# Performance work log

Hardware: AMD Instinct MI355X
Metric: run time of the kernel (lower is better)

Reference implementation:

```python
import jax, jax.numpy as jnp
import numpy as np
from jax import lax

T = 1.0      # terminal time
SIGMA = 1.0  # diffusion coefficient
N, D, P, M, H = 16384, 16, 8, 50, 128


def setup_inputs() -> dict:
    key = jax.random.key(0)
    ks = jax.random.split(key, 8)
    scale1 = 1.0 / np.sqrt(1 + D + P)
    scale2 = 1.0 / np.sqrt(H)
    return {
        "initial_states": jax.random.normal(ks[0], (N, D), jnp.float32),
        "initial_values": jax.random.normal(ks[1], (N,), jnp.float32),
        "observations": jax.random.normal(ks[2], (N, P), jnp.float32),
        "noise": jax.random.normal(ks[3], (M, N, D), jnp.float32),
        "W1": jax.random.normal(ks[4], (1 + D + P, H), jnp.float32) * scale1,
        "b1": jnp.zeros((H,), jnp.float32),
        "W2": jax.random.normal(ks[5], (H, H), jnp.float32) * scale2,
        "b2": jnp.zeros((H,), jnp.float32),
        "W3": jax.random.normal(ks[6], (H, D), jnp.float32) * scale2,
        "b3": jnp.zeros((D,), jnp.float32),
    }


def reference(initial_states, initial_values, observations, noise,
              W1, b1, W2, b2, W3, b3):
    """Euler-Maruyama rollout of simulate_SDEs: joint (X, V) SDE with
    per-step Z-network drift. drift b(X) = -X (OU process)."""
    m_steps = noise.shape[0]
    dt = jnp.asarray(T / m_steps, initial_states.dtype)
    sqrt_dt = jnp.sqrt(dt)
    times = jnp.arange(m_steps, dtype=initial_states.dtype) * dt  # time[m]

    def z_net(t, X, Y):
        tcol = jnp.full((X.shape[0], 1), t, X.dtype)
        h = jnp.concatenate([tcol, X, Y], axis=1)      # (N, 1+d+p)
        h = jax.nn.relu(h @ W1 + b1)
        h = jax.nn.relu(h @ W2 + b2)
        return h @ W3 + b3                             # (N, d)

    def step(carry, inp):
        X, V = carry
        eps, t = inp
        Wn = sqrt_dt * eps                             # Brownian increment
        Z = z_net(t, X, observations)
        drift_V = 0.5 * jnp.sum(Z * Z, axis=1)
        V = V + dt * drift_V + jnp.sum(Z * Wn, axis=1)
        X = X + dt * (-X) + SIGMA * Wn                 # b(X) = -X
        return (X, V), None

    (X, V), _ = lax.scan(step, (initial_states, initial_values), (noise, times))
    return X, V
```

## Files before the change

### kernel.cpp

```cpp
#include <hip/hip_runtime.h>

typedef __bf16   bf16x8 __attribute__((ext_vector_type(8)));
typedef float    f32x4  __attribute__((ext_vector_type(4)));
typedef float    f32x2  __attribute__((ext_vector_type(2)));
typedef uint32_t u32x4  __attribute__((ext_vector_type(4)));

constexpr int N_ = 16384;
constexpr int D_ = 16;
constexpr int P_ = 8;
constexpr int H_ = 128;
constexpr int M_ = 50;

__device__ __forceinline__ uint32_t pk_bf16(float a, float b) {
    uint32_t ua = __builtin_bit_cast(uint32_t, a) + 0x8000u;
    uint32_t ub = __builtin_bit_cast(uint32_t, b) + 0x8000u;
    return __builtin_amdgcn_perm(ub, ua, 0x07060302u);
}
__device__ __forceinline__ uint32_t pk_relu_bf16(float a, float b) {
    return pk_bf16(fmaxf(a, 0.0f), fmaxf(b, 0.0f));
}

__global__ __launch_bounds__(64, 1)
void sde_fused(const float* __restrict__ X0,
               const float* __restrict__ V0,
               const float* __restrict__ Yobs,
               const float* __restrict__ noise,
               const float* __restrict__ W1, const float* __restrict__ b1,
               const float* __restrict__ W2, const float* __restrict__ b2,
               const float* __restrict__ W3, const float* __restrict__ b3,
               float* __restrict__ out)
{
    const int lane = threadIdx.x;
    const int n    = lane & 15;
    const int q    = lane >> 4;
    const int gr   = blockIdx.x * 16 + n;

    const float dt   = 0.02f;
    const float sqdt = 0.1414213562373095f;

    bf16x8 w1f[8];
#pragma unroll
    for (int ct = 0; ct < 8; ++ct) {
        u32x4 u;
        u[0] = pk_bf16(W1[(1 + q * 4 + 0) * H_ + ct * 16 + n],
                       W1[(1 + q * 4 + 1) * H_ + ct * 16 + n]);
        u[1] = pk_bf16(W1[(1 + q * 4 + 2) * H_ + ct * 16 + n],
                       W1[(1 + q * 4 + 3) * H_ + ct * 16 + n]);
        u[2] = pk_bf16(W1[(17 + q * 2 + 0) * H_ + ct * 16 + n],
                       W1[(17 + q * 2 + 1) * H_ + ct * 16 + n]);
        u[3] = (q == 0) ? pk_bf16(b1[ct * 16 + n], W1[ct * 16 + n]) : 0u;
        w1f[ct] = __builtin_bit_cast(bf16x8, u);
    }
    bf16x8 w2f[8][4];
#pragma unroll
    for (int ct = 0; ct < 8; ++ct)
#pragma unroll
        for (int kt = 0; kt < 4; ++kt) {
            u32x4 u;
#pragma unroll
            for (int w = 0; w < 4; ++w) {
                int h0 = (kt * 2 + (w >> 1)) * 16 + q * 4 + (w & 1) * 2;
                u[w] = pk_bf16(W2[h0 * H_ + ct * 16 + n],
                               W2[(h0 + 1) * H_ + ct * 16 + n]);
            }
            w2f[ct][kt] = __builtin_bit_cast(bf16x8, u);
        }
    bf16x8 w3f[4];
#pragma unroll
    for (int kt = 0; kt < 4; ++kt) {
        u32x4 u;
#pragma unroll
        for (int w = 0; w < 4; ++w) {
            int h0 = (kt * 2 + (w >> 1)) * 16 + q * 4 + (w & 1) * 2;
            u[w] = pk_bf16(W3[h0 * D_ + n], W3[(h0 + 1) * D_ + n]);
        }
        w3f[kt] = __builtin_bit_cast(bf16x8, u);
    }
    f32x4 b2r[8];
#pragma unroll
    for (int ct = 0; ct < 8; ++ct)
#pragma unroll
        for (int r = 0; r < 4; ++r) b2r[ct][r] = b2[ct * 16 + q * 4 + r];
    f32x4 b3r;
#pragma unroll
    for (int r = 0; r < 4; ++r) b3r[r] = b3[q * 4 + r];

    f32x4 x = *(const f32x4*)&X0[gr * D_ + q * 4];
    f32x2 y2 = *(const f32x2*)&Yobs[gr * P_ + q * 2];
    const uint32_t yw = pk_bf16(y2[0], y2[1]);

    const float* npb = noise + (size_t)gr * D_ + q * 4;
    f32x4 e0 = *(const f32x4*)npb;
    f32x4 e1 = *(const f32x4*)(npb + (size_t)N_ * D_);
    float t = 0.0f;
    float vacc = 0.0f;

    for (int m = 0; m < M_; ++m) {
        int mp = (m + 2 < M_) ? (m + 2) : (M_ - 1);
        f32x4 e2 = *(const f32x4*)(npb + (size_t)mp * N_ * D_);

        u32x4 au;
        au[0] = pk_bf16(x[0], x[1]);
        au[1] = pk_bf16(x[2], x[3]);
        au[2] = yw;
        au[3] = (q == 0) ? pk_bf16(1.0f, t) : 0u;
        bf16x8 a0 = __builtin_bit_cast(bf16x8, au);

        f32x4 h1c[8];
#pragma unroll
        for (int ct = 0; ct < 8; ++ct)
            h1c[ct] = __builtin_amdgcn_mfma_f32_16x16x32_bf16(
                w1f[ct], a0, (f32x4){0.f, 0.f, 0.f, 0.f}, 0, 0, 0);

        bf16x8 h1b[4];
#pragma unroll
        for (int kt = 0; kt < 4; ++kt) {
            u32x4 u;
            u[0] = pk_relu_bf16(h1c[2 * kt][0], h1c[2 * kt][1]);
            u[1] = pk_relu_bf16(h1c[2 * kt][2], h1c[2 * kt][3]);
            u[2] = pk_relu_bf16(h1c[2 * kt + 1][0], h1c[2 * kt + 1][1]);
            u[3] = pk_relu_bf16(h1c[2 * kt + 1][2], h1c[2 * kt + 1][3]);
            h1b[kt] = __builtin_bit_cast(bf16x8, u);
        }

        f32x4 h2c[8];
#pragma unroll
        for (int ct = 0; ct < 8; ++ct) {
            f32x4 c = b2r[ct];
#pragma unroll
            for (int kt = 0; kt < 4; ++kt)
                c = __builtin_amdgcn_mfma_f32_16x16x32_bf16(w2f[ct][kt], h1b[kt], c, 0, 0, 0);
            h2c[ct] = c;
        }
        bf16x8 h2b[4];
#pragma unroll
        for (int kt = 0; kt < 4; ++kt) {
            u32x4 u;
            u[0] = pk_relu_bf16(h2c[2 * kt][0], h2c[2 * kt][1]);
            u[1] = pk_relu_bf16(h2c[2 * kt][2], h2c[2 * kt][3]);
            u[2] = pk_relu_bf16(h2c[2 * kt + 1][0], h2c[2 * kt + 1][1]);
            u[3] = pk_relu_bf16(h2c[2 * kt + 1][2], h2c[2 * kt + 1][3]);
            h2b[kt] = __builtin_bit_cast(bf16x8, u);
        }

        f32x4 za = __builtin_amdgcn_mfma_f32_16x16x32_bf16(w3f[0], h2b[0], b3r, 0, 0, 0);
        za = __builtin_amdgcn_mfma_f32_16x16x32_bf16(w3f[1], h2b[1], za, 0, 0, 0);
        f32x4 zb = __builtin_amdgcn_mfma_f32_16x16x32_bf16(
            w3f[2], h2b[2], (f32x4){0.f, 0.f, 0.f, 0.f}, 0, 0, 0);
        zb = __builtin_amdgcn_mfma_f32_16x16x32_bf16(w3f[3], h2b[3], zb, 0, 0, 0);

#pragma unroll
        for (int r = 0; r < 4; ++r) {
            float z  = za[r] + zb[r];
            float wn = sqdt * e0[r];
            vacc = fmaf(z, wn, fmaf(0.01f * z, z, vacc));
            x[r] = fmaf(x[r], 0.98f, wn);
        }

        e0 = e1; e1 = e2;
        t += dt;
    }

    float part = vacc;
    part += __shfl_xor(part, 16);
    part += __shfl_xor(part, 32);
    float v = V0[gr] + part;

    *(f32x4*)&out[gr * D_ + q * 4] = x;
    if (q == 0) out[N_ * D_ + gr] = v;
}

extern "C" void kernel_launch(void* const* d_in, const int* in_sizes, int n_in,
                              void* d_out, int out_size, void* d_ws, size_t ws_size,
                              hipStream_t stream)
{
    const float* X0 = (const float*)d_in[0];
    const float* V0 = (const float*)d_in[1];
    const float* Y  = (const float*)d_in[2];
    const float* nz = (const float*)d_in[3];
    const float* W1 = (const float*)d_in[4];
    const float* b1 = (const float*)d_in[5];
    const float* W2 = (const float*)d_in[6];
    const float* b2 = (const float*)d_in[7];
    const float* W3 = (const float*)d_in[8];
    const float* b3 = (const float*)d_in[9];
    float* out = (float*)d_out;

    sde_fused<<<N_ / 16, 64, 0, stream>>>(X0, V0, Y, nz, W1, b1, W2, b2, W3, b3, out);
}
```

Measured before the change: 139.6 us.

## Interleave two Euler steps per iteration to overlap independent MFMA chains

Because the state update does not depend on the network output, the next step's state is computed up front. The MLPs for two consecutive timesteps are then issued together, giving the MFMA pipeline two independent dependency chains to hide latency with only one wave per block. It also replaces the manual bias-add bf16 packing with the hardware v_cvt_pk_bf16_f32 instruction. Costs include higher register use and slightly different rounding.

```diff
diff --git a/kernel.cpp b/kernel.cpp
--- a/kernel.cpp
+++ b/kernel.cpp
@@ -16,8 +16,13 @@
     uint32_t ub = __builtin_bit_cast(uint32_t, b) + 0x8000u;
     return __builtin_amdgcn_perm(ub, ua, 0x07060302u);
 }
-__device__ __forceinline__ uint32_t pk_relu_bf16(float a, float b) {
-    return pk_bf16(fmaxf(a, 0.0f), fmaxf(b, 0.0f));
+__device__ __forceinline__ uint32_t cvtpk(float a, float b) {
+    uint32_t r;
+    asm("v_cvt_pk_bf16_f32 %0, %1, %2" : "=v"(r) : "v"(a), "v"(b));
+    return r;
+}
+__device__ __forceinline__ uint32_t cvtpk_relu(float a, float b) {
+    return cvtpk(fmaxf(a, 0.0f), fmaxf(b, 0.0f));
 }
 
 __global__ __launch_bounds__(64, 1)
@@ -92,76 +97,131 @@
     const float* npb = noise + (size_t)gr * D_ + q * 4;
     f32x4 e0 = *(const f32x4*)npb;
     f32x4 e1 = *(const f32x4*)(npb + (size_t)N_ * D_);
-    float t = 0.0f;
-    float vacc = 0.0f;
-
-    for (int m = 0; m < M_; ++m) {
-        int mp = (m + 2 < M_) ? (m + 2) : (M_ - 1);
-        f32x4 e2 = *(const f32x4*)(npb + (size_t)mp * N_ * D_);
-
-        u32x4 au;
-        au[0] = pk_bf16(x[0], x[1]);
-        au[1] = pk_bf16(x[2], x[3]);
-        au[2] = yw;
-        au[3] = (q == 0) ? pk_bf16(1.0f, t) : 0u;
-        bf16x8 a0 = __builtin_bit_cast(bf16x8, au);
-
-        f32x4 h1c[8];
+    float vaccA = 0.0f, vaccB = 0.0f;
+
+#pragma unroll 1
+    for (int mm = 0; mm < M_; mm += 2) {
+        const int p0 = (mm + 2 < M_) ? (mm + 2) : (M_ - 1);
+        const int p1 = (mm + 3 < M_) ? (mm + 3) : (M_ - 1);
+        f32x4 eN0 = *(const f32x4*)(npb + (size_t)p0 * N_ * D_);
+        f32x4 eN1 = *(const f32x4*)(npb + (size_t)p1 * N_ * D_);
+
+        const float tA = (float)mm * dt;
+        const float tB = (float)(mm + 1) * dt;
+
+        f32x4 xB;
+#pragma unroll
+        for (int r = 0; r < 4; ++r) xB[r] = fmaf(x[r], 0.98f, sqdt * e0[r]);
+
+        u32x4 auA;
+        auA[0] = cvtpk(x[0], x[1]);
+        auA[1] = cvtpk(x[2], x[3]);
+        auA[2] = yw;
+        auA[3] = (q == 0) ? cvtpk(1.0f, tA) : 0u;
+        bf16x8 a0A = __builtin_bit_cast(bf16x8, auA);
+        u32x4 auB;
+        auB[0] = cvtpk(xB[0], xB[1]);
+        auB[1] = cvtpk(xB[2], xB[3]);
+        auB[2] = yw;
+        auB[3] = (q == 0) ? cvtpk(1.0f, tB) : 0u;
+        bf16x8 a0B = __builtin_bit_cast(bf16x8, auB);
+
+        f32x4 h1cA[8], h1cB[8];
 #pragma unroll
         for (int ct = 0; ct < 8; ++ct)
-            h1c[ct] = __builtin_amdgcn_mfma_f32_16x16x32_bf16(
-                w1f[ct], a0, (f32x4){0.f, 0.f, 0.f, 0.f}, 0, 0, 0);
-
-        bf16x8 h1b[4];
-#pragma unroll
-        for (int kt = 0; kt < 4; ++kt) {
-            u32x4 u;
-            u[0] = pk_relu_bf16(h1c[2 * kt][0], h1c[2 * kt][1]);
-            u[1] = pk_relu_bf16(h1c[2 * kt][2], h1c[2 * kt][3]);
-            u[2] = pk_relu_bf16(h1c[2 * kt + 1][0], h1c[2 * kt + 1][1]);
-            u[3] = pk_relu_bf16(h1c[2 * kt + 1][2], h1c[2 * kt + 1][3]);
-            h1b[kt] = __builtin_bit_cast(bf16x8, u);
-        }
-
-        f32x4 h2c[8];
+            h1cA[ct] = __builtin_amdgcn_mfma_f32_16x16x32_bf16(
+                w1f[ct], a0A, (f32x4){0.f, 0.f, 0.f, 0.f}, 0, 0, 0);
+#pragma unroll
+        for (int ct = 0; ct < 8; ++ct)
+            h1cB[ct] = __builtin_amdgcn_mfma_f32_16x16x32_bf16(
+                w1f[ct], a0B, (f32x4){0.f, 0.f, 0.f, 0.f}, 0, 0, 0);
+
+        bf16x8 h1bA[4], h1bB[4];
+#pragma unroll
+        for (int kt = 0; kt < 4; ++kt) {
+            u32x4 u;
+            u[0] = cvtpk_relu(h1cA[2 * kt][0], h1cA[2 * kt][1]);
+            u[1] = cvtpk_relu(h1cA[2 * kt][2], h1cA[2 * kt][3]);
+            u[2] = cvtpk_relu(h1cA[2 * kt + 1][0], h1cA[2 * kt + 1][1]);
+            u[3] = cvtpk_relu(h1cA[2 * kt + 1][2], h1cA[2 * kt + 1][3]);
+            h1bA[kt] = __builtin_bit_cast(bf16x8, u);
+        }
+#pragma unroll
+        for (int kt = 0; kt < 4; ++kt) {
+            u32x4 u;
+            u[0] = cvtpk_relu(h1cB[2 * kt][0], h1cB[2 * kt][1]);
+            u[1] = cvtpk_relu(h1cB[2 * kt][2], h1cB[2 * kt][3]);
+            u[2] = cvtpk_relu(h1cB[2 * kt + 1][0], h1cB[2 * kt + 1][1]);
+            u[3] = cvtpk_relu(h1cB[2 * kt + 1][2], h1cB[2 * kt + 1][3]);
+            h1bB[kt] = __builtin_bit_cast(bf16x8, u);
+        }
+
+        f32x4 h2cA[8], h2cB[8];
 #pragma unroll
         for (int ct = 0; ct < 8; ++ct) {
             f32x4 c = b2r[ct];
 #pragma unroll
             for (int kt = 0; kt < 4; ++kt)
-                c = __builtin_amdgcn_mfma_f32_16x16x32_bf16(w2f[ct][kt], h1b[kt], c, 0, 0, 0);
-            h2c[ct] = c;
-        }
-        bf16x8 h2b[4];
-#pragma unroll
-        for (int kt = 0; kt < 4; ++kt) {
-            u32x4 u;
-            u[0] = pk_relu_bf16(h2c[2 * kt][0], h2c[2 * kt][1]);
-            u[1] = pk_relu_bf16(h2c[2 * kt][2], h2c[2 * kt][3]);
-            u[2] = pk_relu_bf16(h2c[2 * kt + 1][0], h2c[2 * kt + 1][1]);
-            u[3] = pk_relu_bf16(h2c[2 * kt + 1][2], h2c[2 * kt + 1][3]);
-            h2b[kt] = __builtin_bit_cast(bf16x8, u);
-        }
-
-        f32x4 za = __builtin_amdgcn_mfma_f32_16x16x32_bf16(w3f[0], h2b[0], b3r, 0, 0, 0);
-        za = __builtin_amdgcn_mfma_f32_16x16x32_bf16(w3f[1], h2b[1], za, 0, 0, 0);
-        f32x4 zb = __builtin_amdgcn_mfma_f32_16x16x32_bf16(
-            w3f[2], h2b[2], (f32x4){0.f, 0.f, 0.f, 0.f}, 0, 0, 0);
-        zb = __builtin_amdgcn_mfma_f32_16x16x32_bf16(w3f[3], h2b[3], zb, 0, 0, 0);
+                c = __builtin_amdgcn_mfma_f32_16x16x32_bf16(
+                    w2f[ct][kt], h1bA[kt], c, 0, 0, 0);
+            h2cA[ct] = c;
+        }
+#pragma unroll
+        for (int ct = 0; ct < 8; ++ct) {
+            f32x4 c = b2r[ct];
+#pragma unroll
+            for (int kt = 0; kt < 4; ++kt)
+                c = __builtin_amdgcn_mfma_f32_16x16x32_bf16(
+                    w2f[ct][kt], h1bB[kt], c, 0, 0, 0);
+            h2cB[ct] = c;
+        }
+
+        bf16x8 h2bA[4], h2bB[4];
+#pragma unroll
+        for (int kt = 0; kt < 4; ++kt) {
+            u32x4 u;
+            u[0] = cvtpk_relu(h2cA[2 * kt][0], h2cA[2 * kt][1]);
+            u[1] = cvtpk_relu(h2cA[2 * kt][2], h2cA[2 * kt][3]);
+            u[2] = cvtpk_relu(h2cA[2 * kt + 1][0], h2cA[2 * kt + 1][1]);
+            u[3] = cvtpk_relu(h2cA[2 * kt + 1][2], h2cA[2 * kt + 1][3]);
+            h2bA[kt] = __builtin_bit_cast(bf16x8, u);
+        }
+#pragma unroll
+        for (int kt = 0; kt < 4; ++kt) {
+            u32x4 u;
+            u[0] = cvtpk_relu(h2cB[2 * kt][0], h2cB[2 * kt][1]);
+            u[1] = cvtpk_relu(h2cB[2 * kt][2], h2cB[2 * kt][3]);
+            u[2] = cvtpk_relu(h2cB[2 * kt + 1][0], h2cB[2 * kt + 1][1]);
+            u[3] = cvtpk_relu(h2cB[2 * kt + 1][2], h2cB[2 * kt + 1][3]);
+            h2bB[kt] = __builtin_bit_cast(bf16x8, u);
+        }
+
+        f32x4 zaA = __builtin_amdgcn_mfma_f32_16x16x32_bf16(w3f[0], h2bA[0], b3r, 0, 0, 0);
+        zaA = __builtin_amdgcn_mfma_f32_16x16x32_bf16(w3f[1], h2bA[1], zaA, 0, 0, 0);
+        f32x4 zbA = __builtin_amdgcn_mfma_f32_16x16x32_bf16(
+            w3f[2], h2bA[2], (f32x4){0.f, 0.f, 0.f, 0.f}, 0, 0, 0);
+        zbA = __builtin_amdgcn_mfma_f32_16x16x32_bf16(w3f[3], h2bA[3], zbA, 0, 0, 0);
+        f32x4 zaB = __builtin_amdgcn_mfma_f32_16x16x32_bf16(w3f[0], h2bB[0], b3r, 0, 0, 0);
+        zaB = __builtin_amdgcn_mfma_f32_16x16x32_bf16(w3f[1], h2bB[1], zaB, 0, 0, 0);
+        f32x4 zbB = __builtin_amdgcn_mfma_f32_16x16x32_bf16(
+            w3f[2], h2bB[2], (f32x4){0.f, 0.f, 0.f, 0.f}, 0, 0, 0);
+        zbB = __builtin_amdgcn_mfma_f32_16x16x32_bf16(w3f[3], h2bB[3], zbB, 0, 0, 0);
 
 #pragma unroll
         for (int r = 0; r < 4; ++r) {
-            float z  = za[r] + zb[r];
-            float wn = sqdt * e0[r];
-            vacc = fmaf(z, wn, fmaf(0.01f * z, z, vacc));
-            x[r] = fmaf(x[r], 0.98f, wn);
-        }
-
-        e0 = e1; e1 = e2;
-        t += dt;
+            float zA  = zaA[r] + zbA[r];
+            float wnA = sqdt * e0[r];
+            vaccA = fmaf(zA, wnA, fmaf(0.01f * zA, zA, vaccA));
+            float zB  = zaB[r] + zbB[r];
+            float wnB = sqdt * e1[r];
+            vaccB = fmaf(zB, wnB, fmaf(0.01f * zB, zB, vaccB));
+            x[r] = fmaf(xB[r], 0.98f, wnB);
+        }
+
+        e0 = eN0; e1 = eN1;
     }
 
-    float part = vacc;
+    float part = vaccA + vaccB;
     part += __shfl_xor(part, 16);
     part += __shfl_xor(part, 32);
     float v = V0[gr] + part;
```

Result: slower. 156.6 us (+12.2%).

## Stage W1/W3/b2 in LDS, interleave layer-2/3 MFMAs, use hardware bf16 convert

Applied to the files above, without the earlier changes.

Moves the W1 and W3 fragments and the b2 bias out of registers into shared memory and reloads them each step through volatile LDS reads just after use, so fewer values stay live. Layer-2 output is converted and fed into layer-3 MFMAs pair by pair instead of after all eight column tiles. Replaces the manual bit-rounding pack with the v_cvt_pk_bf16_f32 instruction and drops the two-step-ahead noise prefetch in favour of a load inside the non-unrolled loop. The aim is lower register pressure and better MFMA/convert overlap, at the cost of extra LDS traffic and noise-load latency now sitting on the per-step critical path.

```diff
diff --git a/kernel.cpp b/kernel.cpp
--- a/kernel.cpp
+++ b/kernel.cpp
@@ -16,8 +16,22 @@
     uint32_t ub = __builtin_bit_cast(uint32_t, b) + 0x8000u;
     return __builtin_amdgcn_perm(ub, ua, 0x07060302u);
 }
-__device__ __forceinline__ uint32_t pk_relu_bf16(float a, float b) {
-    return pk_bf16(fmaxf(a, 0.0f), fmaxf(b, 0.0f));
+__device__ __forceinline__ uint32_t cvtpk(float a, float b) {
+    uint32_t r;
+    asm("v_cvt_pk_bf16_f32 %0, %1, %2" : "=v"(r) : "v"(a), "v"(b));
+    return r;
+}
+__device__ __forceinline__ uint32_t cvtpk_relu(float a, float b) {
+    return cvtpk(fmaxf(a, 0.0f), fmaxf(b, 0.0f));
+}
+
+__device__ __forceinline__ bf16x8 lds_ldv8(const void* p) {
+    u32x4 v = *(volatile const u32x4*)p;
+    return __builtin_bit_cast(bf16x8, v);
+}
+__device__ __forceinline__ f32x4 lds_ldvf(const void* p) {
+    u32x4 v = *(volatile const u32x4*)p;
+    return __builtin_bit_cast(f32x4, v);
 }
 
 __global__ __launch_bounds__(64, 1)
@@ -38,7 +52,10 @@
     const float dt   = 0.02f;
     const float sqdt = 0.1414213562373095f;
 
-    bf16x8 w1f[8];
+    __shared__ bf16x8 w1s[8][64];
+    __shared__ bf16x8 w3s[4][64];
+    __shared__ float  b2s[H_];
+
 #pragma unroll
     for (int ct = 0; ct < 8; ++ct) {
         u32x4 u;
@@ -49,11 +66,23 @@
         u[2] = pk_bf16(W1[(17 + q * 2 + 0) * H_ + ct * 16 + n],
                        W1[(17 + q * 2 + 1) * H_ + ct * 16 + n]);
         u[3] = (q == 0) ? pk_bf16(b1[ct * 16 + n], W1[ct * 16 + n]) : 0u;
-        w1f[ct] = __builtin_bit_cast(bf16x8, u);
-    }
+        w1s[ct][lane] = __builtin_bit_cast(bf16x8, u);
+    }
+#pragma unroll
+    for (int kt = 0; kt < 4; ++kt) {
+        u32x4 u;
+#pragma unroll
+        for (int w = 0; w < 4; ++w) {
+            int h0 = (kt * 2 + (w >> 1)) * 16 + q * 4 + (w & 1) * 2;
+            u[w] = pk_bf16(W3[h0 * D_ + n], W3[(h0 + 1) * D_ + n]);
+        }
+        w3s[kt][lane] = __builtin_bit_cast(bf16x8, u);
+    }
+    if (lane < 32) *(f32x4*)&b2s[lane * 4] = *(const f32x4*)&b2[lane * 4];
+
     bf16x8 w2f[8][4];
 #pragma unroll
-    for (int ct = 0; ct < 8; ++ct)
+    for (int ct = 0; ct < 8; ++ct) {
 #pragma unroll
         for (int kt = 0; kt < 4; ++kt) {
             u32x4 u;
@@ -65,99 +94,102 @@
             }
             w2f[ct][kt] = __builtin_bit_cast(bf16x8, u);
         }
-    bf16x8 w3f[4];
-#pragma unroll
-    for (int kt = 0; kt < 4; ++kt) {
-        u32x4 u;
-#pragma unroll
-        for (int w = 0; w < 4; ++w) {
-            int h0 = (kt * 2 + (w >> 1)) * 16 + q * 4 + (w & 1) * 2;
-            u[w] = pk_bf16(W3[h0 * D_ + n], W3[(h0 + 1) * D_ + n]);
-        }
-        w3f[kt] = __builtin_bit_cast(bf16x8, u);
-    }
-    f32x4 b2r[8];
-#pragma unroll
-    for (int ct = 0; ct < 8; ++ct)
-#pragma unroll
-        for (int r = 0; r < 4; ++r) b2r[ct][r] = b2[ct * 16 + q * 4 + r];
-    f32x4 b3r;
-#pragma unroll
-    for (int r = 0; r < 4; ++r) b3r[r] = b3[q * 4 + r];
+        __builtin_amdgcn_sched_barrier(0);
+    }
+    f32x4 b3r = *(const f32x4*)&b3[q * 4];
+
+    __syncthreads();
 
     f32x4 x = *(const f32x4*)&X0[gr * D_ + q * 4];
     f32x2 y2 = *(const f32x2*)&Yobs[gr * P_ + q * 2];
     const uint32_t yw = pk_bf16(y2[0], y2[1]);
-
     const float* npb = noise + (size_t)gr * D_ + q * 4;
-    f32x4 e0 = *(const f32x4*)npb;
-    f32x4 e1 = *(const f32x4*)(npb + (size_t)N_ * D_);
+
+    bf16x8 w1buf[8];
+#pragma unroll
+    for (int k = 0; k < 8; ++k) w1buf[k] = lds_ldv8(&w1s[k][lane]);
+    bf16x8 w3buf[4];
+#pragma unroll
+    for (int k = 0; k < 4; ++k) w3buf[k] = lds_ldv8(&w3s[k][lane]);
+    f32x4 cb[4];
+    cb[0] = lds_ldvf(&b2s[0 * 16 + q * 4]);
+    cb[1] = lds_ldvf(&b2s[1 * 16 + q * 4]);
+
     float t = 0.0f;
     float vacc = 0.0f;
 
+#pragma unroll 1
     for (int m = 0; m < M_; ++m) {
-        int mp = (m + 2 < M_) ? (m + 2) : (M_ - 1);
-        f32x4 e2 = *(const f32x4*)(npb + (size_t)mp * N_ * D_);
+        f32x4 e = *(const f32x4*)(npb + (size_t)m * N_ * D_);
 
         u32x4 au;
-        au[0] = pk_bf16(x[0], x[1]);
-        au[1] = pk_bf16(x[2], x[3]);
+        au[0] = cvtpk(x[0], x[1]);
+        au[1] = cvtpk(x[2], x[3]);
         au[2] = yw;
-        au[3] = (q == 0) ? pk_bf16(1.0f, t) : 0u;
+        au[3] = (q == 0) ? cvtpk(1.0f, t) : 0u;
         bf16x8 a0 = __builtin_bit_cast(bf16x8, au);
 
-        f32x4 h1c[8];
-#pragma unroll
-        for (int ct = 0; ct < 8; ++ct)
-            h1c[ct] = __builtin_amdgcn_mfma_f32_16x16x32_bf16(
-                w1f[ct], a0, (f32x4){0.f, 0.f, 0.f, 0.f}, 0, 0, 0);
-
         bf16x8 h1b[4];
 #pragma unroll
         for (int kt = 0; kt < 4; ++kt) {
+            f32x4 ha = __builtin_amdgcn_mfma_f32_16x16x32_bf16(
+                w1buf[2 * kt], a0, (f32x4){0.f, 0.f, 0.f, 0.f}, 0, 0, 0);
+            f32x4 hb = __builtin_amdgcn_mfma_f32_16x16x32_bf16(
+                w1buf[2 * kt + 1], a0, (f32x4){0.f, 0.f, 0.f, 0.f}, 0, 0, 0);
+            w1buf[2 * kt]     = lds_ldv8(&w1s[2 * kt][lane]);
+            w1buf[2 * kt + 1] = lds_ldv8(&w1s[2 * kt + 1][lane]);
             u32x4 u;
-            u[0] = pk_relu_bf16(h1c[2 * kt][0], h1c[2 * kt][1]);
-            u[1] = pk_relu_bf16(h1c[2 * kt][2], h1c[2 * kt][3]);
-            u[2] = pk_relu_bf16(h1c[2 * kt + 1][0], h1c[2 * kt + 1][1]);
-            u[3] = pk_relu_bf16(h1c[2 * kt + 1][2], h1c[2 * kt + 1][3]);
+            u[0] = cvtpk_relu(ha[0], ha[1]);
+            u[1] = cvtpk_relu(ha[2], ha[3]);
+            u[2] = cvtpk_relu(hb[0], hb[1]);
+            u[3] = cvtpk_relu(hb[2], hb[3]);
             h1b[kt] = __builtin_bit_cast(bf16x8, u);
         }
 
-        f32x4 h2c[8];
+        f32x4 za, zb, hprev;
 #pragma unroll
         for (int ct = 0; ct < 8; ++ct) {
-            f32x4 c = b2r[ct];
+            cb[(ct + 2) & 3] = lds_ldvf(&b2s[((ct + 2) & 7) * 16 + q * 4]);
+            f32x4 c = cb[ct & 3];
 #pragma unroll
             for (int kt = 0; kt < 4; ++kt)
-                c = __builtin_amdgcn_mfma_f32_16x16x32_bf16(w2f[ct][kt], h1b[kt], c, 0, 0, 0);
-            h2c[ct] = c;
-        }
-        bf16x8 h2b[4];
-#pragma unroll
-        for (int kt = 0; kt < 4; ++kt) {
-            u32x4 u;
-            u[0] = pk_relu_bf16(h2c[2 * kt][0], h2c[2 * kt][1]);
-            u[1] = pk_relu_bf16(h2c[2 * kt][2], h2c[2 * kt][3]);
-            u[2] = pk_relu_bf16(h2c[2 * kt + 1][0], h2c[2 * kt + 1][1]);
-            u[3] = pk_relu_bf16(h2c[2 * kt + 1][2], h2c[2 * kt + 1][3]);
-            h2b[kt] = __builtin_bit_cast(bf16x8, u);
-        }
-
-        f32x4 za = __builtin_amdgcn_mfma_f32_16x16x32_bf16(w3f[0], h2b[0], b3r, 0, 0, 0);
-        za = __builtin_amdgcn_mfma_f32_16x16x32_bf16(w3f[1], h2b[1], za, 0, 0, 0);
-        f32x4 zb = __builtin_amdgcn_mfma_f32_16x16x32_bf16(
-            w3f[2], h2b[2], (f32x4){0.f, 0.f, 0.f, 0.f}, 0, 0, 0);
-        zb = __builtin_amdgcn_mfma_f32_16x16x32_bf16(w3f[3], h2b[3], zb, 0, 0, 0);
+                c = __builtin_amdgcn_mfma_f32_16x16x32_bf16(
+                    w2f[ct][kt], h1b[kt], c, 0, 0, 0);
+            if ((ct & 1) == 0) {
+                hprev = c;
+            } else {
+                u32x4 u;
+                u[0] = cvtpk_relu(hprev[0], hprev[1]);
+                u[1] = cvtpk_relu(hprev[2], hprev[3]);
+                u[2] = cvtpk_relu(c[0], c[1]);
+                u[3] = cvtpk_relu(c[2], c[3]);
+                bf16x8 h2b = __builtin_bit_cast(bf16x8, u);
+                const int j = ct >> 1;
+                if (j == 0) {
+                    za = __builtin_amdgcn_mfma_f32_16x16x32_bf16(w3buf[0], h2b, b3r, 0, 0, 0);
+                    w3buf[0] = lds_ldv8(&w3s[0][lane]);
+                } else if (j == 1) {
+                    za = __builtin_amdgcn_mfma_f32_16x16x32_bf16(w3buf[1], h2b, za, 0, 0, 0);
+                    w3buf[1] = lds_ldv8(&w3s[1][lane]);
+                } else if (j == 2) {
+                    zb = __builtin_amdgcn_mfma_f32_16x16x32_bf16(
+                        w3buf[2], h2b, (f32x4){0.f, 0.f, 0.f, 0.f}, 0, 0, 0);
+                    w3buf[2] = lds_ldv8(&w3s[2][lane]);
+                } else {
+                    zb = __builtin_amdgcn_mfma_f32_16x16x32_bf16(w3buf[3], h2b, zb, 0, 0, 0);
+                    w3buf[3] = lds_ldv8(&w3s[3][lane]);
+                }
+            }
+        }
 
 #pragma unroll
         for (int r = 0; r < 4; ++r) {
             float z  = za[r] + zb[r];
-            float wn = sqdt * e0[r];
+            float wn = sqdt * e[r];
             vacc = fmaf(z, wn, fmaf(0.01f * z, z, vacc));
             x[r] = fmaf(x[r], 0.98f, wn);
         }
 
-        e0 = e1; e1 = e2;
         t += dt;
     }
 
```

New measurement: 173.5 us. 24.3% more time.
